# Kernel tuning notes

Hardware: AMD Instinct MI355X
Metric: run time of the kernel (lower is better)

The kernel has to match this reference:

```python
import jax, jax.numpy as jnp
import numpy as np

# Config mirrors Model(d_model=512, output_dim=2); RetNet(num_layers=2, n_heads=1)
D_MODEL = 512
N_LAYERS = 2
OUT_DIM = 2
B, S = 16, 1024
GAMMA = 1.0 - 2.0 ** -5  # RetNet decay for head 0 (n_heads=1)
EPS = 1e-6


def setup_inputs() -> dict:
    key = jax.random.key(0)
    ks = jax.random.split(key, 10)
    d, L = D_MODEL, N_LAYERS

    def rn(k, shape, scale):
        return jax.random.normal(k, shape, dtype=jnp.float32) * scale

    return {
        "x": rn(ks[0], (B, S, d), 1.0),
        # per-layer retention projections, stacked on a leading layer axis
        "Wq": rn(ks[1], (L, d, d), d ** -0.5),
        "Wk": rn(ks[2], (L, d, d), d ** -0.5),
        "Wv": rn(ks[3], (L, d, d), d ** -0.5),
        "Wg": rn(ks[4], (L, d, d), d ** -0.5),
        "Wo": rn(ks[5], (L, d, d), d ** -0.5),
        # pre-norm LayerNorm affine params
        "ln1_g": jnp.ones((L, d), jnp.float32),
        "ln1_b": jnp.zeros((L, d), jnp.float32),
        "ln2_g": jnp.ones((L, d), jnp.float32),
        "ln2_b": jnp.zeros((L, d), jnp.float32),
        # FFN (hidden = 2*d_model, gelu) per RetNet paper
        "W1": rn(ks[6], (L, d, 2 * d), d ** -0.5),
        "b1": jnp.zeros((L, 2 * d), jnp.float32),
        "W2": rn(ks[7], (L, 2 * d, d), (2 * d) ** -0.5),
        "b2": jnp.zeros((L, d), jnp.float32),
        # readout Linear(d_model, output_dim)
        "Wro": rn(ks[8], (d, OUT_DIM), d ** -0.5),
        "bro": jnp.zeros((OUT_DIM,), jnp.float32),
    }


def _layer_norm(x, g, b):
    mu = jnp.mean(x, axis=-1, keepdims=True)
    var = jnp.var(x, axis=-1, keepdims=True)
    return (x - mu) * jax.lax.rsqrt(var + EPS) * g + b


def _retention(x, Wq, Wk, Wv, Wg, Wo):
    # single head: d_head = d_model
    d = x.shape[-1]
    q = x @ Wq                      # [B,S,d]
    k = (x @ Wk) * (d ** -0.5)      # scaled keys
    v = x @ Wv
    n = jnp.arange(x.shape[1])
    diff = n[:, None] - n[None, :]
    # D[n,m] = gamma^(n-m) for n >= m else 0 (causal decay mask)
    D = jnp.where(diff >= 0, jnp.exp(diff.astype(jnp.float32) * np.log(GAMMA)), 0.0)
    scores = jnp.einsum("bnd,bmd->bnm", q, k) * D       # [B,S,S]
    ret = jnp.einsum("bnm,bmd->bnd", scores, v)          # [B,S,d]
    # GroupNorm over the (single) head dim, no affine
    mu = jnp.mean(ret, axis=-1, keepdims=True)
    var = jnp.var(ret, axis=-1, keepdims=True)
    ret = (ret - mu) * jax.lax.rsqrt(var + EPS)
    # swish gate + output projection
    return (jax.nn.silu(x @ Wg) * ret) @ Wo


def reference(x, Wq, Wk, Wv, Wg, Wo, ln1_g, ln1_b, ln2_g, ln2_b, W1, b1, W2, b2, Wro, bro):
    h = x
    for l in range(N_LAYERS):  # small fixed layer count
        h = h + _retention(_layer_norm(h, ln1_g[l], ln1_b[l]), Wq[l], Wk[l], Wv[l], Wg[l], Wo[l])
        y = _layer_norm(h, ln2_g[l], ln2_b[l])
        h = h + jax.nn.gelu(y @ W1[l] + b1[l]) @ W2[l] + b2[l]
    pooled = h.sum(axis=1)          # [B,d] sum pooling over sequence
    return pooled @ Wro + bro       # [B,OUT_DIM]
```

## Files before the change

### kernel.cpp

```cpp
#include <hip/hip_runtime.h>
#include <hip/hip_bf16.h>


#define D_MODEL 512
#define SEQ 1024
#define BATCH 16
#define NROWS (BATCH * SEQ)
#define HID 1024
#define LOG2_GAMMA (-0.04580368961f)
#define KSCALE (0.044194173824f)

typedef __attribute__((ext_vector_type(8))) short bf16x8;
typedef __attribute__((ext_vector_type(4))) float f32x4;

__device__ inline unsigned short f2bf(float x) {
    union { float f; unsigned u; } uu; uu.f = x;
    unsigned r = uu.u + 0x7fff + ((uu.u >> 16) & 1);
    return (unsigned short)(r >> 16);
}
__device__ inline float bf2f(unsigned short x) {
    union { unsigned u; float f; } uu; uu.u = ((unsigned)x) << 16; return uu.f;
}

__device__ inline void gload_lds16(const void* g, void* l) {
    __builtin_amdgcn_global_load_lds(
        (const __attribute__((address_space(1))) void*)g,
        (__attribute__((address_space(3))) void*)l, 16, 0, 0);
}

__device__ inline float sigm(float z) {
    return 1.f / (1.f + exp2f(z * -1.442695040888963f));
}
__device__ inline float gelu_fast(float x) {
    float y = 1.5957691216057308f * (x + 0.044715f * x * x * x);
    return x * sigm(y);
}

template <int EPI>
__global__ __launch_bounds__(512, 2) void gemm256p(
    const short* __restrict__ A, const short* __restrict__ B,
    const float* __restrict__ bias, unsigned short* __restrict__ C,
    int K, int lda, int ldb, int ldc, int nbx) {
    __shared__ __align__(16) short smem[4 * 16384];
    const int tid = threadIdx.x;
    const int lane = tid & 63;
    const int wid = tid >> 6;
    const int wm = wid >> 2, wn = wid & 3;
    const int cpx = gridDim.x >> 3;
    const int wg = ((int)blockIdx.x & 7) * cpx + ((int)blockIdx.x >> 3);
    const int m0 = (wg / nbx) * 256;
    const int n0 = (wg % nbx) * 256;

    const int srow = tid >> 2;
    const int scol = (((tid & 3) ^ ((tid >> 3) & 3)) * 8);
    auto stage = [&](int slot, int t) {
        int k0 = t * 32;
#pragma unroll
        for (int r = 0; r < 2; ++r) {
            gload_lds16(A + (long long)(m0 + r * 128 + srow) * lda + k0 + scol,
                        &smem[slot * 16384 + r * 4096 + wid * 512]);
            gload_lds16(B + (long long)(n0 + r * 128 + srow) * ldb + k0 + scol,
                        &smem[slot * 16384 + 8192 + r * 4096 + wid * 512]);
        }
    };

    const int NT = K >> 5;
    f32x4 acc[8][4] = {};
    const int sw8 = (((lane >> 4) ^ ((lane >> 1) & 3)) * 8);
    const int aoff = (wm * 128 + (lane & 15)) * 32 + sw8;
    const int boff = 8192 + (wn * 64 + (lane & 15)) * 32 + sw8;

    bf16x8 aR0[8], bR0[4], aR1[8], bR1[4];
    stage(0, 0); stage(1, 1); stage(2, 2);
    asm volatile("s_waitcnt vmcnt(8)" ::: "memory");
    __builtin_amdgcn_s_barrier();
#pragma unroll
    for (int m = 0; m < 8; ++m) aR0[m] = *(const bf16x8*)&smem[aoff + m * 512];
#pragma unroll
    for (int n = 0; n < 4; ++n) bR0[n] = *(const bf16x8*)&smem[boff + n * 512];

#define STEP256(T, AC, BC, AN, BN2)                                                   \
    {                                                                                 \
        int t = (T);                                                                  \
        if (t + 3 < NT) stage((t + 3) & 3, t + 3);                                    \
        if (t + 3 < NT)      asm volatile("s_waitcnt vmcnt(8)" ::: "memory");         \
        else if (t + 2 < NT) asm volatile("s_waitcnt vmcnt(4)" ::: "memory");         \
        else if (t + 1 < NT) asm volatile("s_waitcnt vmcnt(0)" ::: "memory");         \
        __builtin_amdgcn_s_barrier();                                                 \
        const int sb = ((t + 1) & 3) * 16384;                                         \
        const bool pre = (t + 1 < NT);                                                \
        _Pragma("unroll")                                                             \
        for (int q = 0; q < 4; ++q) {                                                 \
            if (pre) {                                                                \
                AN[2 * q] = *(const bf16x8*)&smem[sb + aoff + (2 * q) * 512];          \
                AN[2 * q + 1] = *(const bf16x8*)&smem[sb + aoff + (2 * q + 1) * 512];  \
                BN2[q] = *(const bf16x8*)&smem[sb + boff + q * 512];                   \
            }                                                                         \
            __builtin_amdgcn_s_setprio(1);                                            \
            _Pragma("unroll")                                                         \
            for (int n = 0; n < 4; ++n) {                                             \
                acc[2 * q][n] = __builtin_amdgcn_mfma_f32_16x16x32_bf16(AC[2 * q], BC[n], acc[2 * q][n], 0, 0, 0); \
                acc[2 * q + 1][n] = __builtin_amdgcn_mfma_f32_16x16x32_bf16(AC[2 * q + 1], BC[n], acc[2 * q + 1][n], 0, 0, 0); \
            }                                                                         \
            __builtin_amdgcn_s_setprio(0);                                            \
            __builtin_amdgcn_sched_barrier(0);                                        \
        }                                                                             \
        asm volatile("s_waitcnt lgkmcnt(0)" ::: "memory");                            \
        __builtin_amdgcn_sched_barrier(0);                                            \
    }

    for (int tt = 0; tt < NT; tt += 2) {
        STEP256(tt, aR0, bR0, aR1, bR1)
        STEP256(tt + 1, aR1, bR1, aR0, bR0)
    }
#undef STEP256

    const int ocol = lane & 15;
    const int orow4 = (lane >> 4) * 4;
    float bv[4];
    if (EPI == 2) {
#pragma unroll
        for (int n = 0; n < 4; ++n) bv[n] = bias[n0 + wn * 64 + n * 16 + ocol];
    }
#pragma unroll 1
    for (int half = 0; half < 2; ++half) {
        __syncthreads();
        if (wm == half) {
#pragma unroll
            for (int m = 0; m < 8; ++m)
#pragma unroll
                for (int n = 0; n < 4; ++n)
#pragma unroll
                    for (int rj = 0; rj < 4; ++rj) {
                        int lr = m * 16 + orow4 + rj;
                        int lc = wn * 64 + n * 16 + ocol;
                        float v = acc[m][n][rj];
                        if (EPI == 2) v = gelu_fast(v + bv[n]);
                        smem[lr * 256 + lc] = (short)f2bf(v);
                    }
        }
        __syncthreads();
#pragma unroll
        for (int p = 0; p < 8; ++p) {
            int s = p * 512 + tid;
            int row = s >> 5;
            int cc = (s & 31) * 8;
            *(int4*)&C[(long long)(m0 + half * 128 + row) * ldc + n0 + cc] =
                *(const int4*)&smem[row * 256 + cc];
        }
    }
}

template <int EPI>
__global__ __launch_bounds__(256, 4) void pgemm64(
    const short* __restrict__ A, const short* __restrict__ B,
    const float* __restrict__ bias, unsigned short* __restrict__ C,
    int K, int lda, int ldb, int ldc,
    long long sA, long long sB, long long sC, int tri) {
    __shared__ __align__(16) short smem[4 * 6144];
    const int tid = threadIdx.x;
    const int lane = tid & 63;
    const int wid = tid >> 6;
    const int wr = wid;
    const int m0 = blockIdx.y * 128, n0 = blockIdx.x * 64;
    A += (long long)blockIdx.z * sA;
    B += (long long)blockIdx.z * sB;

    int Keff = K;
    if (tri) { int km = m0 + 128; if (km < Keff) Keff = km; }
    const int NT = Keff >> 5;

    auto stage = [&](int slot, int t) {
        int k0 = t * 32;
#pragma unroll
        for (int it = 0; it < 2; ++it) {
            int c = it * 256 + tid;
            int rr = c >> 2;
            int cc = ((c & 3) ^ ((c >> 3) & 3)) * 8;
            gload_lds16(A + (long long)(m0 + rr) * lda + k0 + cc,
                        &smem[slot * 6144 + (it * 256 + wid * 64) * 8]);
        }
        {
            int c = tid;
            int rr = c >> 2;
            int cc = ((c & 3) ^ ((c >> 3) & 3)) * 8;
            gload_lds16(B + (long long)(n0 + rr) * ldb + k0 + cc,
                        &smem[slot * 6144 + 4096 + (wid * 64) * 8]);
        }
    };

    f32x4 acc[2][4] = {};
    const int sw8 = (((lane >> 4) ^ ((lane >> 1) & 3)) * 8);
    const int aoff = (wr * 32 + (lane & 15)) * 32 + sw8;
    const int boff = 4096 + ((lane & 15)) * 32 + sw8;

    bf16x8 aR0[2], bR0[4], aR1[2], bR1[4];
    stage(0, 0); stage(1, 1); stage(2, 2);
    asm volatile("s_waitcnt vmcnt(6)" ::: "memory");
    __builtin_amdgcn_s_barrier();
#pragma unroll
    for (int m = 0; m < 2; ++m) aR0[m] = *(const bf16x8*)&smem[aoff + m * 512];
#pragma unroll
    for (int n = 0; n < 4; ++n) bR0[n] = *(const bf16x8*)&smem[boff + n * 512];

#define STEP64(T, AC, BC, AN, BN2)                                                    \
    {                                                                                 \
        int t = (T);                                                                  \
        if (t + 3 < NT) stage((t + 3) & 3, t + 3);                                    \
        if (t + 3 < NT)      asm volatile("s_waitcnt vmcnt(6)" ::: "memory");         \
        else if (t + 2 < NT) asm volatile("s_waitcnt vmcnt(3)" ::: "memory");         \
        else if (t + 1 < NT) asm volatile("s_waitcnt vmcnt(0)" ::: "memory");         \
        __builtin_amdgcn_s_barrier();                                                 \
        const int sb = ((t + 1) & 3) * 6144;                                          \
        const bool pre = (t + 1 < NT);                                                \
        _Pragma("unroll")                                                             \
        for (int q = 0; q < 2; ++q) {                                                 \
            if (pre) {                                                                \
                AN[q] = *(const bf16x8*)&smem[sb + aoff + q * 512];                    \
                BN2[2 * q] = *(const bf16x8*)&smem[sb + boff + (2 * q) * 512];         \
                BN2[2 * q + 1] = *(const bf16x8*)&smem[sb + boff + (2 * q + 1) * 512]; \
            }                                                                         \
            __builtin_amdgcn_s_setprio(1);                                            \
            _Pragma("unroll")                                                         \
            for (int m = 0; m < 2; ++m) {                                             \
                acc[m][2 * q] = __builtin_amdgcn_mfma_f32_16x16x32_bf16(AC[m], BC[2 * q], acc[m][2 * q], 0, 0, 0); \
                acc[m][2 * q + 1] = __builtin_amdgcn_mfma_f32_16x16x32_bf16(AC[m], BC[2 * q + 1], acc[m][2 * q + 1], 0, 0, 0); \
            }                                                                         \
            __builtin_amdgcn_s_setprio(0);                                            \
            __builtin_amdgcn_sched_barrier(0);                                        \
        }                                                                             \
        asm volatile("s_waitcnt lgkmcnt(0)" ::: "memory");                            \
        __builtin_amdgcn_sched_barrier(0);                                            \
    }

    for (int tt = 0; tt < NT; tt += 2) {
        STEP64(tt, aR0, bR0, aR1, bR1)
        STEP64(tt + 1, aR1, bR1, aR0, bR0)
    }
#undef STEP64

    __syncthreads();
    const int orow = (lane >> 4) * 4;
    const int ocol = lane & 15;
    float bv[4];
    if (EPI >= 1) {
#pragma unroll
        for (int j = 0; j < 4; ++j) bv[j] = bias[n0 + j * 16 + ocol];
    }
#pragma unroll
    for (int i = 0; i < 2; ++i)
#pragma unroll
        for (int j = 0; j < 4; ++j)
#pragma unroll
            for (int rj = 0; rj < 4; ++rj) {
                int lrow = wr * 32 + i * 16 + orow + rj;
                int lcol = j * 16 + ocol;
                float val = acc[i][j][rj];
                if (EPI == 1) val += bv[j];
                if (EPI == 2) val = gelu_fast(val + bv[j]);
                smem[lrow * 64 + lcol] = (short)f2bf(val);
            }
    __syncthreads();
    const long long zoff = (long long)blockIdx.z * sC;
#pragma unroll
    for (int p = 0; p < 4; ++p) {
        int s = p * 256 + tid;
        int row = s >> 3;
        int cc = (s & 7) * 8;
        *(int4*)&C[zoff + (long long)(m0 + row) * ldc + n0 + cc] = *(const int4*)&smem[row * 64 + cc];
    }
}

__global__ __launch_bounds__(256, 2) void pdecay(
    const short* __restrict__ Q, const short* __restrict__ Kp,
    unsigned short* __restrict__ S, int lda, long long sA) {
    if (blockIdx.x > blockIdx.y) return;
    const int q0 = blockIdx.y * 128;
    const int c0 = blockIdx.x * 128;
    unsigned short* Sb = S + (long long)blockIdx.z * SEQ * SEQ;
    __shared__ __align__(16) short smem[4 * 8192];
    const int tid = threadIdx.x;
    const int lane = tid & 63;
    const int wid = tid >> 6;
    const int wr = wid >> 1, wc = wid & 1;
    const short* Ab = Q + (long long)blockIdx.z * sA;
    const short* Bb = Kp + (long long)blockIdx.z * sA;

    auto stage = [&](int slot, int t) {
        int k0 = t * 32;
#pragma unroll
        for (int it = 0; it < 2; ++it) {
            int c = it * 256 + tid;
            int rr = c >> 2;
            int cc = ((c & 3) ^ ((c >> 3) & 3)) * 8;
            gload_lds16(Ab + (long long)(q0 + rr) * lda + k0 + cc,
                        &smem[slot * 8192 + (it * 256 + wid * 64) * 8]);
            gload_lds16(Bb + (long long)(c0 + rr) * lda + k0 + cc,
                        &smem[slot * 8192 + 4096 + (it * 256 + wid * 64) * 8]);
        }
    };

    const int NT = D_MODEL / 32;
    f32x4 acc[4][4] = {};
    const int sw8 = (((lane >> 4) ^ ((lane >> 1) & 3)) * 8);
    const int aoff = (wr * 64 + (lane & 15)) * 32 + sw8;
    const int boff = 4096 + (wc * 64 + (lane & 15)) * 32 + sw8;

    bf16x8 aR0[4], bR0[4], aR1[4], bR1[4];
    stage(0, 0); stage(1, 1); stage(2, 2);
    asm volatile("s_waitcnt vmcnt(8)" ::: "memory");
    __builtin_amdgcn_s_barrier();
#pragma unroll
    for (int m = 0; m < 4; ++m) aR0[m] = *(const bf16x8*)&smem[aoff + m * 512];
#pragma unroll
    for (int n = 0; n < 4; ++n) bR0[n] = *(const bf16x8*)&smem[boff + n * 512];

#define STEPD(T, AC, BC, AN, BN2)                                                     \
    {                                                                                 \
        int t = (T);                                                                  \
        if (t + 3 < NT) stage((t + 3) & 3, t + 3);                                    \
        if (t + 3 < NT)      asm volatile("s_waitcnt vmcnt(8)" ::: "memory");         \
        else if (t + 2 < NT) asm volatile("s_waitcnt vmcnt(4)" ::: "memory");         \
        else if (t + 1 < NT) asm volatile("s_waitcnt vmcnt(0)" ::: "memory");         \
        __builtin_amdgcn_s_barrier();                                                 \
        const int sb = ((t + 1) & 3) * 8192;                                          \
        const bool pre = (t + 1 < NT);                                                \
        _Pragma("unroll")                                                             \
        for (int q = 0; q < 4; ++q) {                                                 \
            if (pre) {                                                                \
                AN[q] = *(const bf16x8*)&smem[sb + aoff + q * 512];                    \
                BN2[q] = *(const bf16x8*)&smem[sb + boff + q * 512];                   \
            }                                                                         \
            __builtin_amdgcn_s_setprio(1);                                            \
            _Pragma("unroll")                                                         \
            for (int n = 0; n < 4; ++n)                                               \
                acc[q][n] = __builtin_amdgcn_mfma_f32_16x16x32_bf16(AC[q], BC[n], acc[q][n], 0, 0, 0); \
            __builtin_amdgcn_s_setprio(0);                                            \
            __builtin_amdgcn_sched_barrier(0);                                        \
        }                                                                             \
        asm volatile("s_waitcnt lgkmcnt(0)" ::: "memory");                            \
        __builtin_amdgcn_sched_barrier(0);                                            \
    }

    for (int tt = 0; tt < NT; tt += 2) {
        STEPD(tt, aR0, bR0, aR1, bR1)
        STEPD(tt + 1, aR1, bR1, aR0, bR0)
    }
#undef STEPD

    __syncthreads();
    const int orow = (lane >> 4) * 4;
    const int ocol = lane & 15;
#pragma unroll
    for (int i = 0; i < 4; ++i)
#pragma unroll
        for (int j = 0; j < 4; ++j)
#pragma unroll
            for (int rj = 0; rj < 4; ++rj) {
                int lrow = wr * 64 + i * 16 + orow + rj;
                int lcol = wc * 64 + j * 16 + ocol;
                int n = q0 + lrow, m = c0 + lcol;
                float w = (n >= m) ? exp2f((float)(n - m) * LOG2_GAMMA) * KSCALE : 0.f;
                smem[lrow * 128 + lcol] = (short)f2bf(acc[i][j][rj] * w);
            }
    __syncthreads();
#pragma unroll
    for (int p = 0; p < 8; ++p) {
        int s = p * 256 + tid;
        int row = s >> 4;
        int cc = (s & 15) * 8;
        *(int4*)&Sb[(long long)(q0 + row) * SEQ + c0 + cc] = *(const int4*)&smem[row * 128 + cc];
    }
}

__global__ __launch_bounds__(256) void wconv_all(
    const float* __restrict__ Wq, const float* __restrict__ Wk,
    const float* __restrict__ Wv, const float* __restrict__ Wg,
    const float* __restrict__ Wo, const float* __restrict__ W1,
    const float* __restrict__ W2,
    unsigned short* __restrict__ WqkvgT, unsigned short* __restrict__ WoT,
    unsigned short* __restrict__ W1T, unsigned short* __restrict__ W2T) {
    const long long dd = 512LL * 512;
    int z = blockIdx.z;
    int l = z / 7, w = z % 7;
    const float* src; unsigned short* dst; int K, N;
    switch (w) {
        case 0: src = Wq + l * dd; dst = WqkvgT + (long long)l * 4 * dd; K = 512; N = 512; break;
        case 1: src = Wk + l * dd; dst = WqkvgT + (long long)l * 4 * dd + dd; K = 512; N = 512; break;
        case 2: src = Wv + l * dd; dst = WqkvgT + (long long)l * 4 * dd + 2 * dd; K = 512; N = 512; break;
        case 3: src = Wg + l * dd; dst = WqkvgT + (long long)l * 4 * dd + 3 * dd; K = 512; N = 512; break;
        case 4: src = Wo + l * dd; dst = WoT + l * dd; K = 512; N = 512; break;
        case 5: src = W1 + (long long)l * 512 * 1024; dst = W1T + (long long)l * 512 * 1024; K = 512; N = 1024; break;
        default: src = W2 + (long long)l * 1024 * 512; dst = W2T + (long long)l * 1024 * 512; K = 1024; N = 512; break;
    }
    if ((int)blockIdx.x >= N / 64 || (int)blockIdx.y >= K / 64) return;
    __shared__ unsigned short t[64][65];
    int n0 = blockIdx.x * 64, k0 = blockIdx.y * 64;
    int tx = threadIdx.x & 63, ty = threadIdx.x >> 6;
#pragma unroll
    for (int i = 0; i < 16; ++i)
        t[ty + i * 4][tx] = f2bf(src[(long long)(k0 + ty + i * 4) * N + n0 + tx]);
    __syncthreads();
#pragma unroll
    for (int i = 0; i < 16; ++i)
        dst[(long long)(n0 + ty + i * 4) * K + k0 + tx] = t[tx][ty + i * 4];
}

__global__ __launch_bounds__(256) void vtrans(const unsigned short* __restrict__ in,
                                              unsigned short* __restrict__ out, int istride) {
    __shared__ unsigned short t[64][65];
    const unsigned short* pin = in + (long long)blockIdx.z * SEQ * istride;
    unsigned short* pout = out + (long long)blockIdx.z * D_MODEL * SEQ;
    int c0 = blockIdx.x * 64, r0 = blockIdx.y * 64;
    int tx = threadIdx.x & 63, ty = threadIdx.x >> 6;
#pragma unroll
    for (int i = 0; i < 16; ++i)
        t[ty + i * 4][tx] = pin[(long long)(r0 + ty + i * 4) * istride + c0 + tx];
    __syncthreads();
#pragma unroll
    for (int i = 0; i < 16; ++i)
        pout[(long long)(c0 + ty + i * 4) * SEQ + r0 + tx] = t[tx][ty + i * 4];
}

template <int MODE>
__global__ __launch_bounds__(256) void ln_fuse(
    const void* __restrict__ hin_v,
    const unsigned short* __restrict__ delta,
    const float* __restrict__ g, const float* __restrict__ b,
    unsigned short* __restrict__ hout,
    unsigned short* __restrict__ y) {
    int row = blockIdx.x * 4 + (threadIdx.x >> 6);
    int t = threadIdx.x & 63;
    float f[8];
    if (MODE == 2) {
        const float4* r4 = (const float4*)((const float*)hin_v + (long long)row * D_MODEL);
        float4 v0 = r4[2 * t], v1 = r4[2 * t + 1];
        f[0] = v0.x; f[1] = v0.y; f[2] = v0.z; f[3] = v0.w;
        f[4] = v1.x; f[5] = v1.y; f[6] = v1.z; f[7] = v1.w;
    } else {
        const unsigned short* hin = (const unsigned short*)hin_v;
        int4 hv = ((const int4*)(hin + (long long)row * D_MODEL))[t];
        const unsigned short* hu = (const unsigned short*)&hv;
#pragma unroll
        for (int k = 0; k < 8; ++k) f[k] = bf2f(hu[k]);
    }
    if (MODE == 1) {
        int4 dv = ((const int4*)(delta + (long long)row * D_MODEL))[t];
        const unsigned short* du = (const unsigned short*)&dv;
#pragma unroll
        for (int k = 0; k < 8; ++k) f[k] += bf2f(du[k]);
    }
    float s = 0.f, s2 = 0.f;
#pragma unroll
    for (int k = 0; k < 8; ++k) { s += f[k]; s2 += f[k] * f[k]; }
#pragma unroll
    for (int off = 32; off > 0; off >>= 1) {
        s += __shfl_down(s, off);
        s2 += __shfl_down(s2, off);
    }
    s = __shfl(s, 0); s2 = __shfl(s2, 0);
    float mu = s * (1.f / D_MODEL);
    float var = s2 * (1.f / D_MODEL) - mu * mu;
    float rs = rsqrtf(var + 1e-6f);
    if (MODE >= 1) {
        ushort4 ho[2];
        unsigned short* hp = (unsigned short*)ho;
#pragma unroll
        for (int k = 0; k < 8; ++k) hp[k] = f2bf(f[k]);
        ((int4*)(hout + (long long)row * D_MODEL))[t] = *(int4*)ho;
    }
    const float4* g4 = (const float4*)g;
    const float4* b4 = (const float4*)b;
    float4 ga = g4[2 * t], gb2 = g4[2 * t + 1];
    float4 ba = b4[2 * t], bb2 = b4[2 * t + 1];
    float gg[8] = {ga.x, ga.y, ga.z, ga.w, gb2.x, gb2.y, gb2.z, gb2.w};
    float bb[8] = {ba.x, ba.y, ba.z, ba.w, bb2.x, bb2.y, bb2.z, bb2.w};
    ushort4 yo[2];
    unsigned short* yp = (unsigned short*)yo;
#pragma unroll
    for (int k = 0; k < 8; ++k) yp[k] = f2bf((f[k] - mu) * rs * gg[k] + bb[k]);
    ((int4*)(y + (long long)row * D_MODEL))[t] = *(int4*)yo;
}

__global__ __launch_bounds__(256) void gate_bf16(const unsigned short* __restrict__ ret,
                                                 const unsigned short* __restrict__ g,
                                                 int gstride,
                                                 unsigned short* __restrict__ out) {
    int row = blockIdx.x * 4 + (threadIdx.x >> 6);
    int t = threadIdx.x & 63;
    int4 rv4 = ((const int4*)(ret + (long long)row * D_MODEL))[t];
    const unsigned short* ru = (const unsigned short*)&rv4;
    float f[8];
#pragma unroll
    for (int k = 0; k < 8; ++k) f[k] = bf2f(ru[k]);
    float s = 0.f, s2 = 0.f;
#pragma unroll
    for (int k = 0; k < 8; ++k) { s += f[k]; s2 += f[k] * f[k]; }
#pragma unroll
    for (int off = 32; off > 0; off >>= 1) {
        s += __shfl_down(s, off);
        s2 += __shfl_down(s2, off);
    }
    s = __shfl(s, 0); s2 = __shfl(s2, 0);
    float mu = s * (1.f / D_MODEL);
    float var = s2 * (1.f / D_MODEL) - mu * mu;
    float rs = rsqrtf(var + 1e-6f);
    int4 gv4 = ((const int4*)(g + (long long)row * gstride))[t];
    const unsigned short* gu = (const unsigned short*)&gv4;
    ushort4 o[2];
    unsigned short* op = (unsigned short*)o;
#pragma unroll
    for (int k = 0; k < 8; ++k) {
        float x = bf2f(gu[k]);
        op[k] = f2bf(x * sigm(x) * (f[k] - mu) * rs);
    }
    ((int4*)(out + (long long)row * D_MODEL))[t] = *(int4*)o;
}

__global__ __launch_bounds__(256) void pool_s1(const unsigned short* __restrict__ h,
                                               const unsigned short* __restrict__ d,
                                               float* __restrict__ partial) {
    int b = blockIdx.x >> 4, g = blockIdx.x & 15;
    long long base = ((long long)b * SEQ + g * 64) * D_MODEL;
    int cw = (threadIdx.x & 63) * 8;
    int rg = threadIdx.x >> 6;
    float a[8] = {};
    for (int r = rg; r < 64; r += 4) {
        long long o = base + (long long)r * D_MODEL + cw;
        int4 hv = *(const int4*)&h[o];
        int4 dv = *(const int4*)&d[o];
        const unsigned short* hp = (const unsigned short*)&hv;
        const unsigned short* dp = (const unsigned short*)&dv;
#pragma unroll
        for (int j = 0; j < 8; ++j) a[j] += bf2f(hp[j]) + bf2f(dp[j]);
    }
    __shared__ float red[4][512];
#pragma unroll
    for (int j = 0; j < 8; ++j) red[rg][cw + j] = a[j];
    __syncthreads();
#pragma unroll
    for (int cc = 0; cc < 2; ++cc) {
        int c = threadIdx.x * 2 + cc;
        partial[(long long)blockIdx.x * D_MODEL + c] =
            red[0][c] + red[1][c] + red[2][c] + red[3][c];
    }
}

__global__ __launch_bounds__(256) void pool_s2(const float* __restrict__ partial,
                                               float* __restrict__ pooled) {
    int idx = blockIdx.x * 256 + threadIdx.x;
    int b = idx >> 9, c = idx & 511;
    float s = 0.f;
#pragma unroll
    for (int g = 0; g < 16; ++g) s += partial[(long long)(b * 16 + g) * D_MODEL + c];
    pooled[idx] = s;
}

__global__ __launch_bounds__(64) void readout_kernel(const float* __restrict__ pooled,
                                                     const float* __restrict__ Wro,
                                                     const float* __restrict__ bro,
                                                     float* __restrict__ out) {
    int bo = blockIdx.x;
    int b = bo >> 1, o = bo & 1;
    int t = threadIdx.x;
    float s = 0.f;
    for (int i = t; i < D_MODEL; i += 64) s += pooled[b * D_MODEL + i] * Wro[i * 2 + o];
#pragma unroll
    for (int off = 32; off > 0; off >>= 1) s += __shfl_down(s, off);
    if (t == 0) out[b * 2 + o] = s + bro[o];
}

extern "C" void kernel_launch(void* const* d_in, const int* in_sizes, int n_in,
                              void* d_out, int out_size, void* d_ws, size_t ws_size,
                              hipStream_t stream) {
    const float* x = (const float*)d_in[0];
    const float* Wq = (const float*)d_in[1];
    const float* Wk = (const float*)d_in[2];
    const float* Wv = (const float*)d_in[3];
    const float* Wg = (const float*)d_in[4];
    const float* Wo = (const float*)d_in[5];
    const float* ln1_g = (const float*)d_in[6];
    const float* ln1_b = (const float*)d_in[7];
    const float* ln2_g = (const float*)d_in[8];
    const float* ln2_b = (const float*)d_in[9];
    const float* W1 = (const float*)d_in[10];
    const float* b1 = (const float*)d_in[11];
    const float* W2 = (const float*)d_in[12];
    const float* b2 = (const float*)d_in[13];
    const float* Wro = (const float*)d_in[14];
    const float* bro = (const float*)d_in[15];
    float* out = (float*)d_out;

    const long long NE = (long long)NROWS * D_MODEL;
    const long long dd = (long long)D_MODEL * D_MODEL;

    unsigned short* h = (unsigned short*)d_ws;
    unsigned short* y = h + NE;
    unsigned short* qkvg = y + NE;
    unsigned short* vT = qkvg + 4 * NE;
    unsigned short* gated = vT;
    unsigned short* ret = vT + NE;
    unsigned short* sg = ret + NE;
    float* pooled = (float*)(sg + 2 * NE);
    float* partial = pooled + 8192;
    unsigned short* wts = (unsigned short*)(partial + 256 * 512);
    unsigned short* WqkvgT = wts;
    unsigned short* WoT = WqkvgT + 2 * 4 * dd;
    unsigned short* W1T = WoT + 2 * dd;
    unsigned short* W2T = W1T + 2 * (long long)D_MODEL * HID;

    dim3 blk(256);
    wconv_all<<<dim3(16, 16, 14), blk, 0, stream>>>(Wq, Wk, Wv, Wg, Wo, W1, W2,
                                                    WqkvgT, WoT, W1T, W2T);

    for (int l = 0; l < 2; l++) {
        if (l == 0)
            ln_fuse<2><<<NROWS / 4, blk, 0, stream>>>(x, nullptr, ln1_g, ln1_b, h, y);
        else
            ln_fuse<1><<<NROWS / 4, blk, 0, stream>>>(h, ret, ln1_g + l * D_MODEL,
                                                      ln1_b + l * D_MODEL, h, y);
        gemm256p<0><<<512, 512, 0, stream>>>(
            (const short*)y, (const short*)(WqkvgT + (long long)l * 4 * dd), nullptr, qkvg,
            512, 512, 512, 2048, 8);
        vtrans<<<dim3(8, 16, BATCH), blk, 0, stream>>>(qkvg + 1024, vT, 2048);
        pdecay<<<dim3(8, 8, BATCH), blk, 0, stream>>>(
            (const short*)qkvg, (const short*)(qkvg + 512), sg, 2048, (long long)SEQ * 2048);
        pgemm64<0><<<dim3(8, 8, BATCH), blk, 0, stream>>>(
            (const short*)sg, (const short*)vT, nullptr, ret,
            SEQ, SEQ, SEQ, 512,
            (long long)SEQ * SEQ, (long long)D_MODEL * SEQ, (long long)SEQ * D_MODEL, 1);
        gate_bf16<<<NROWS / 4, blk, 0, stream>>>(ret, qkvg + 1536, 2048, gated);
        pgemm64<0><<<dim3(8, 128), blk, 0, stream>>>(
            (const short*)gated, (const short*)(WoT + l * dd), nullptr, sg,
            512, 512, 512, 512, 0, 0, 0, 0);
        ln_fuse<1><<<NROWS / 4, blk, 0, stream>>>(h, sg, ln2_g + l * D_MODEL,
                                                  ln2_b + l * D_MODEL, h, y);
        gemm256p<2><<<256, 512, 0, stream>>>(
            (const short*)y, (const short*)(W1T + (long long)l * D_MODEL * HID),
            b1 + l * HID, sg, 512, 512, 512, HID, 4);
        pgemm64<1><<<dim3(8, 128), blk, 0, stream>>>(
            (const short*)sg, (const short*)(W2T + (long long)l * HID * D_MODEL),
            b2 + l * D_MODEL, ret, HID, HID, HID, 512, 0, 0, 0, 0);
    }

    pool_s1<<<256, blk, 0, stream>>>(h, ret, partial);
    pool_s2<<<32, blk, 0, stream>>>(partial, pooled);
    readout_kernel<<<32, 64, 0, stream>>>(pooled, Wro, bro, out);
}
```

Baseline: 526.6 us.

## Band-limit decayed retention and fuse V transpose into QKVG GEMM epilogue

The causal decay mask is truncated to a band of four 128-wide key blocks. pdecay skips score tiles more than three blocks below the diagonal, and the score×V GEMM starts its K loop at m0-384. This relies on gamma^384 being about 5e-6, which is negligible at bf16 precision. Separately, the QKVG GEMM now writes the V columns transposed straight from its epilogue through LDS, which removes the standalone vtrans kernel and its global round trip. The band truncation is a numerical approximation that depends on the fixed decay constant, not on the test inputs.

```diff
diff --git a/kernel.cpp b/kernel.cpp
--- a/kernel.cpp
+++ b/kernel.cpp
@@ -36,11 +36,12 @@
     return x * sigm(y);
 }
 
-template <int EPI>
+template <int EPI, int VT>
 __global__ __launch_bounds__(512, 2) void gemm256p(
     const short* __restrict__ A, const short* __restrict__ B,
     const float* __restrict__ bias, unsigned short* __restrict__ C,
-    int K, int lda, int ldb, int ldc, int nbx) {
+    int K, int lda, int ldb, int ldc, int nbx,
+    unsigned short* __restrict__ vTp) {
     __shared__ __align__(16) short smem[4 * 16384];
     const int tid = threadIdx.x;
     const int lane = tid & 63;
@@ -117,6 +118,39 @@
 
     const int ocol = lane & 15;
     const int orow4 = (lane >> 4) * 4;
+    const bool isv = VT && (n0 >= 1024) && (n0 < 1536);
+    if (isv) {
+        const int dbase = n0 - 1024;
+        const int b = m0 >> 10;
+        const int s0g = m0 & 1023;
+        unsigned short* vTb = vTp + ((long long)b * 512 + dbase) * 1024 + s0g;
+#pragma unroll 1
+        for (int half = 0; half < 2; ++half) {
+            __syncthreads();
+            if (wm == half) {
+#pragma unroll
+                for (int m = 0; m < 8; ++m)
+#pragma unroll
+                    for (int n = 0; n < 4; ++n)
+#pragma unroll
+                        for (int rj = 0; rj < 4; ++rj) {
+                            int lr = m * 16 + orow4 + rj;
+                            int lc = wn * 64 + n * 16 + ocol;
+                            smem[lc * 136 + lr] = (short)f2bf(acc[m][n][rj]);
+                        }
+            }
+            __syncthreads();
+#pragma unroll
+            for (int p = 0; p < 8; ++p) {
+                int idx = p * 512 + tid;
+                int d = idx >> 4;
+                int s8 = (idx & 15) * 8;
+                *(int4*)&vTb[(long long)d * 1024 + half * 128 + s8] =
+                    *(const int4*)&smem[d * 136 + s8];
+            }
+        }
+        return;
+    }
     float bv[4];
     if (EPI == 2) {
 #pragma unroll
@@ -167,11 +201,13 @@
     B += (long long)blockIdx.z * sB;
 
     int Keff = K;
+    int kstart = 0;
     if (tri) { int km = m0 + 128; if (km < Keff) Keff = km; }
-    const int NT = Keff >> 5;
+    if (tri == 2) { int ks = m0 - 384; if (ks > 0) kstart = ks; }
+    const int NT = (Keff - kstart) >> 5;
 
     auto stage = [&](int slot, int t) {
-        int k0 = t * 32;
+        int k0 = kstart + t * 32;
 #pragma unroll
         for (int it = 0; it < 2; ++it) {
             int c = it * 256 + tid;
@@ -275,6 +311,7 @@
     const short* __restrict__ Q, const short* __restrict__ Kp,
     unsigned short* __restrict__ S, int lda, long long sA) {
     if (blockIdx.x > blockIdx.y) return;
+    if (blockIdx.y > blockIdx.x + 3) return;
     const int q0 = blockIdx.y * 128;
     const int c0 = blockIdx.x * 128;
     unsigned short* Sb = S + (long long)blockIdx.z * SEQ * SEQ;
@@ -406,22 +443,6 @@
         dst[(long long)(n0 + ty + i * 4) * K + k0 + tx] = t[tx][ty + i * 4];
 }
 
-__global__ __launch_bounds__(256) void vtrans(const unsigned short* __restrict__ in,
-                                              unsigned short* __restrict__ out, int istride) {
-    __shared__ unsigned short t[64][65];
-    const unsigned short* pin = in + (long long)blockIdx.z * SEQ * istride;
-    unsigned short* pout = out + (long long)blockIdx.z * D_MODEL * SEQ;
-    int c0 = blockIdx.x * 64, r0 = blockIdx.y * 64;
-    int tx = threadIdx.x & 63, ty = threadIdx.x >> 6;
-#pragma unroll
-    for (int i = 0; i < 16; ++i)
-        t[ty + i * 4][tx] = pin[(long long)(r0 + ty + i * 4) * istride + c0 + tx];
-    __syncthreads();
-#pragma unroll
-    for (int i = 0; i < 16; ++i)
-        pout[(long long)(c0 + ty + i * 4) * SEQ + r0 + tx] = t[tx][ty + i * 4];
-}
-
 template <int MODE>
 __global__ __launch_bounds__(256) void ln_fuse(
     const void* __restrict__ hin_v,
@@ -619,25 +640,24 @@
         else
             ln_fuse<1><<<NROWS / 4, blk, 0, stream>>>(h, ret, ln1_g + l * D_MODEL,
                                                       ln1_b + l * D_MODEL, h, y);
-        gemm256p<0><<<512, 512, 0, stream>>>(
+        gemm256p<0, 1><<<512, 512, 0, stream>>>(
             (const short*)y, (const short*)(WqkvgT + (long long)l * 4 * dd), nullptr, qkvg,
-            512, 512, 512, 2048, 8);
-        vtrans<<<dim3(8, 16, BATCH), blk, 0, stream>>>(qkvg + 1024, vT, 2048);
+            512, 512, 512, 2048, 8, vT);
         pdecay<<<dim3(8, 8, BATCH), blk, 0, stream>>>(
             (const short*)qkvg, (const short*)(qkvg + 512), sg, 2048, (long long)SEQ * 2048);
         pgemm64<0><<<dim3(8, 8, BATCH), blk, 0, stream>>>(
             (const short*)sg, (const short*)vT, nullptr, ret,
             SEQ, SEQ, SEQ, 512,
-            (long long)SEQ * SEQ, (long long)D_MODEL * SEQ, (long long)SEQ * D_MODEL, 1);
+            (long long)SEQ * SEQ, (long long)D_MODEL * SEQ, (long long)SEQ * D_MODEL, 2);
         gate_bf16<<<NROWS / 4, blk, 0, stream>>>(ret, qkvg + 1536, 2048, gated);
         pgemm64<0><<<dim3(8, 128), blk, 0, stream>>>(
             (const short*)gated, (const short*)(WoT + l * dd), nullptr, sg,
             512, 512, 512, 512, 0, 0, 0, 0);
         ln_fuse<1><<<NROWS / 4, blk, 0, stream>>>(h, sg, ln2_g + l * D_MODEL,
                                                   ln2_b + l * D_MODEL, h, y);
-        gemm256p<2><<<256, 512, 0, stream>>>(
+        gemm256p<2, 0><<<256, 512, 0, stream>>>(
             (const short*)y, (const short*)(W1T + (long long)l * D_MODEL * HID),
-            b1 + l * HID, sg, 512, 512, 512, HID, 4);
+            b1 + l * HID, sg, 512, 512, 512, HID, 4, nullptr);
         pgemm64<1><<<dim3(8, 128), blk, 0, stream>>>(
             (const short*)sg, (const short*)(W2T + (long long)l * HID * D_MODEL),
             b2 + l * D_MODEL, ret, HID, HID, HID, 512, 0, 0, 0, 0);
```

Measured after the change: 522.5 us. Within noise of the previous version (-0.8%).
